# Performance work log

Hardware: AMD Instinct MI355X
Metric: run time of the kernel (lower is better)

Reference implementation:

```python
import jax, jax.numpy as jnp
import numpy as np

NUM_CLASSES = 2
OVERLAP_THRESHOLD = 0.35
NEG_POS_RATIO = 7
VARIANCES = (0.1, 0.2)
B, P, G = 16, 131072, 32


def point_form(pri):
    # center form (cx,cy,w,h) -> corner form (x1,y1,x2,y2)
    return jnp.concatenate([pri[:, :2] - pri[:, 2:] / 2,
                            pri[:, :2] + pri[:, 2:] / 2], axis=1)


def jaccard(box_a, box_b):
    # box_a [G,4], box_b [P,4], corner form -> IoU [G,P]
    max_xy = jnp.minimum(box_a[:, None, 2:], box_b[None, :, 2:])
    min_xy = jnp.maximum(box_a[:, None, :2], box_b[None, :, :2])
    inter = jnp.prod(jnp.clip(max_xy - min_xy, 0.0, None), axis=2)
    area_a = jnp.prod(box_a[:, 2:] - box_a[:, :2], axis=1)[:, None]
    area_b = jnp.prod(box_b[:, 2:] - box_b[:, :2], axis=1)[None, :]
    return inter / (area_a + area_b - inter)


def encode(matched, pri, variances):
    g_cxcy = ((matched[:, :2] + matched[:, 2:]) / 2 - pri[:, :2]) / (variances[0] * pri[:, 2:])
    g_wh = jnp.log((matched[:, 2:] - matched[:, :2]) / pri[:, 2:]) / variances[1]
    return jnp.concatenate([g_cxcy, g_wh], axis=1)


def encode_landm(matched, pri, variances):
    m = matched.reshape(-1, 5, 2)  # [P,5,2]
    g = (m - pri[:, None, :2]) / (variances[0] * pri[:, None, 2:])
    return g.reshape(-1, 10)


def match_one(truths, landms, labels, pri):
    overlaps = jaccard(truths, point_form(pri))          # [G,P]
    best_prior_idx = jnp.argmax(overlaps, axis=1)        # [G] best prior per gt
    best_truth_overlap = jnp.max(overlaps, axis=0)       # [P]
    best_truth_idx = jnp.argmax(overlaps, axis=0)        # [P]
    # ensure each gt keeps its best prior
    best_truth_overlap = best_truth_overlap.at[best_prior_idx].set(2.0)
    best_truth_idx = best_truth_idx.at[best_prior_idx].set(jnp.arange(truths.shape[0]))
    matches = truths[best_truth_idx]                     # [P,4]
    conf = jnp.where(best_truth_overlap < OVERLAP_THRESHOLD, 0, labels[best_truth_idx])
    loc = encode(matches, pri, VARIANCES)
    landm = encode_landm(landms[best_truth_idx], pri, VARIANCES)
    return loc, conf, landm


def smooth_l1(pred, gt):
    d = jnp.abs(pred - gt)
    return jnp.where(d < 1.0, 0.5 * d * d, d - 0.5)


def multibox_loss(conf_data, loc_data, landm_data, priors, targets):
    batch_size, num_priors = loc_data.shape[0], priors.shape[0]
    truths = targets[:, :, :4]
    landms = targets[:, :, 4:14]
    labels = targets[:, :, 14].astype(jnp.int32)
    loc_t, conf_t, landm_t = jax.vmap(lambda t, l, lb: match_one(t, l, lb, priors))(truths, landms, labels)

    pos = conf_t > 0                                      # [B,P]
    num_pos_total = jnp.maximum(pos.sum().astype(loc_data.dtype), 1.0)
    num_pos_per_image = pos.sum(axis=1, keepdims=True)    # [B,1]
    posf = pos.astype(loc_data.dtype)

    loss_box = (smooth_l1(loc_data, loc_t).sum(-1) * posf).sum()
    loss_landm = (smooth_l1(landm_data, landm_t).sum(-1) * posf).sum()

    logp = jax.nn.log_softmax(conf_data, axis=-1)         # [B,P,C]
    ce = -jnp.take_along_axis(logp, jnp.clip(conf_t, 0, None)[..., None], axis=-1)[..., 0]
    loss_c = jnp.where(pos | (conf_t < 0), 0.0, ce)       # zero pos & ignored
    # hard negative mining: rank by descending loss via double argsort
    loss_idx = jnp.argsort(-loss_c, axis=1)
    idx_rank = jnp.argsort(loss_idx, axis=1)
    num_neg = jnp.minimum(NEG_POS_RATIO * num_pos_per_image, num_priors - 1)
    neg = idx_rank < num_neg
    pn = (pos | neg).astype(conf_data.dtype)
    loss_c_final = (ce * pn).sum()
    return (loss_box / num_pos_total, loss_c_final / num_pos_total, loss_landm / num_pos_total)


def setup_inputs() -> dict:
    key = jax.random.key(0)
    k1, k2, k3, k4, k5, k6, k7 = jax.random.split(key, 7)
    conf_data = jax.random.normal(k1, (B, P, NUM_CLASSES), dtype=jnp.float32)
    loc_data = jax.random.normal(k2, (B, P, 4), dtype=jnp.float32)
    landm_data = jax.random.normal(k3, (B, P, 10), dtype=jnp.float32)
    # priors in center form
    pc = jax.random.uniform(k4, (P, 2), minval=0.0, maxval=1.0)
    pwh = jax.random.uniform(k5, (P, 2), minval=0.02, maxval=0.3)
    priors = jnp.concatenate([pc, pwh], axis=1).astype(jnp.float32)
    # targets: [B,G,15] = corner box(4) + landms(10) + label(1)
    c = jax.random.uniform(k6, (B, G, 2), minval=0.2, maxval=0.8)
    s = jax.random.uniform(k7, (B, G, 2), minval=0.05, maxval=0.3)
    box = jnp.concatenate([c - s / 2, c + s / 2], axis=-1)
    lm = jax.random.uniform(jax.random.fold_in(key, 99), (B, G, 10), minval=0.0, maxval=1.0)
    lbl = jnp.ones((B, G, 1), dtype=jnp.float32)
    targets = jnp.concatenate([box, lm, lbl], axis=-1).astype(jnp.float32)
    return {"conf_data": conf_data, "loc_data": loc_data, "landm_data": landm_data,
            "priors": priors, "targets": targets}


def reference(conf_data, loc_data, landm_data, priors, targets):
    return multibox_loss(conf_data, loc_data, landm_data, priors, targets)
```

## Files before the change

### kernel.cpp

```cpp
#include <hip/hip_runtime.h>
#include <math.h>

#define B_ 16
#define P_ 131072
#define G_ 32
constexpr float OVER_THR = 0.35f;
constexpr float VAR0 = 0.1f;
constexpr float VAR1 = 0.2f;
constexpr int NEG_POS = 7;
constexpr int UNR = 8;
constexpr int LOSS_X = P_ / 256;
constexpr int LOSS_BLOCKS = LOSS_X * B_;
constexpr int NBIN13 = 8192;
constexpr int NBIN8 = 256;
constexpr int NBIN11 = 2048;
constexpr int SCAN_BLKS = 16;

__device__ inline float s1(float d) {
    d = fabsf(d);
    return d < 1.f ? 0.5f * d * d : d - 0.5f;
}

__device__ inline unsigned long long shfl_xor_u64(unsigned long long x, int m) {
    unsigned lo = (unsigned)x, hi = (unsigned)(x >> 32);
    lo = __shfl_xor(lo, m);
    hi = __shfl_xor(hi, m);
    return ((unsigned long long)hi << 32) | lo;
}

template <int NB>
__device__ void topk_select(const unsigned* __restrict__ h, unsigned rem,
                            int* out_bin, unsigned* out_rem) {
    constexpr int CHUNK = NB / 256;
    const int tid = threadIdx.x;
    unsigned cnt[CHUNK];
    unsigned csum = 0;
#pragma unroll
    for (int j = 0; j < CHUNK; ++j) { cnt[j] = h[tid * CHUNK + j]; csum += cnt[j]; }
    __shared__ unsigned ss[256];
    ss[tid] = csum;
    __syncthreads();
    for (int off = 1; off < 256; off <<= 1) {
        unsigned other = (tid + off < 256) ? ss[tid + off] : 0u;
        __syncthreads();
        ss[tid] += other;
        __syncthreads();
    }
    unsigned incl = ss[tid];
    unsigned excl = incl - csum;
    if (excl < rem && incl >= rem) {
        unsigned r = rem - excl, cum = 0;
        int selbin = tid * CHUNK;
#pragma unroll
        for (int j = CHUNK - 1; j >= 0; --j) {
            unsigned c = cnt[j];
            if (cum + c >= r) { selbin = tid * CHUNK + j; r = r - cum; break; }
            cum += c;
        }
        *out_bin = selbin;
        *out_rem = r;
    }
}

__global__ __launch_bounds__(256, 3) void k_match(
        const float4* __restrict__ priors4, const float* __restrict__ targets,
        float* __restrict__ bt_ov, unsigned char* __restrict__ bt_idx,
        unsigned long long* __restrict__ pack) {
    const int b = blockIdx.y;
    const int base = blockIdx.x * (256 * UNR);
    const int tid = threadIdx.x;
    __shared__ float tb[G_][5];
    __shared__ unsigned long long red[G_][4];
    if (tid < G_ * 4) {
        int g = tid >> 2, j = tid & 3;
        tb[g][j] = targets[((size_t)b * G_ + g) * 15 + j];
    }
    __syncthreads();
    if (tid < G_) tb[tid][4] = (tb[tid][2] - tb[tid][0]) * (tb[tid][3] - tb[tid][1]);
    __syncthreads();

    float px1[UNR], py1[UNR], px2[UNR], py2[UNR], pap[UNR], best[UNR];
    int bidx[UNR];
#pragma unroll
    for (int j = 0; j < UNR; ++j) {
        float4 pr = priors4[base + j * 256 + tid];
        px1[j] = pr.x - pr.z * 0.5f;  py1[j] = pr.y - pr.w * 0.5f;
        px2[j] = pr.x + pr.z * 0.5f;  py2[j] = pr.y + pr.w * 0.5f;
        pap[j] = pr.z * pr.w;
        best[j] = -1.0f; bidx[j] = 0;
    }
    const int lane = tid & 63, wave = tid >> 6;
#pragma unroll 1
    for (int g = 0; g < G_; ++g) {
        float t0 = tb[g][0], t1 = tb[g][1], t2 = tb[g][2], t3 = tb[g][3], ta = tb[g][4];
        float gb = -1.0f; int gj = 0;
#pragma unroll
        for (int j = 0; j < UNR; ++j) {
            float iw = fminf(t2, px2[j]) - fmaxf(t0, px1[j]);
            float ih = fminf(t3, py2[j]) - fmaxf(t1, py1[j]);
            float inter = fmaxf(iw, 0.f) * fmaxf(ih, 0.f);
            float iou = inter * __builtin_amdgcn_rcpf(ta + pap[j] - inter);
            if (iou > best[j]) { best[j] = iou; bidx[j] = g; }
            if (iou > gb) { gb = iou; gj = j; }
        }
        unsigned p = (unsigned)(base + (gj << 8) + tid);
        unsigned long long pk =
            ((unsigned long long)__float_as_uint(gb) << 32) | (unsigned)(~p);
#pragma unroll
        for (int off = 32; off > 0; off >>= 1) {
            unsigned long long o = shfl_xor_u64(pk, off);
            if (o > pk) pk = o;
        }
        if (lane == 0) red[g][wave] = pk;
    }
    __syncthreads();
    if (tid < G_) {
        unsigned long long m = red[tid][0];
#pragma unroll
        for (int w = 1; w < 4; ++w) if (red[tid][w] > m) m = red[tid][w];
        atomicMax(&pack[b * G_ + tid], m);
    }
#pragma unroll
    for (int j = 0; j < UNR; ++j) {
        int p = base + j * 256 + tid;
        size_t o = (size_t)b * P_ + p;
        bt_ov[o] = best[j];
        bt_idx[o] = (unsigned char)bidx[j];
    }
}

__global__ void k_override(const unsigned long long* __restrict__ pack,
                           float* __restrict__ bt_ov, unsigned char* __restrict__ bt_idx) {
    int b = threadIdx.x;
    if (b >= B_) return;
    for (int g = 0; g < G_; ++g) {
        unsigned long long pk = pack[b * G_ + g];
        unsigned p = ~(unsigned)(pk & 0xFFFFFFFFull);
        if (p < P_) {
            bt_ov[(size_t)b * P_ + p] = 2.0f;
            bt_idx[(size_t)b * P_ + p] = (unsigned char)g;
        }
    }
}

__global__ __launch_bounds__(256) void k_loss(
        const float2* __restrict__ conf2, const float4* __restrict__ loc4,
        const float* __restrict__ landm, const float4* __restrict__ priors4,
        const float* __restrict__ targets,
        const float* __restrict__ bt_ov, const unsigned char* __restrict__ bt_idx,
        float* __restrict__ ce_neg,
        double* __restrict__ pb, double* __restrict__ pl,
        double* __restrict__ pc, int* __restrict__ pn) {
    const int b = blockIdx.y;
    const int p = blockIdx.x * 256 + threadIdx.x;
    const int tid = threadIdx.x;
    __shared__ float tg[G_ * 15];
    for (int i = tid; i < G_ * 15; i += 256) tg[i] = targets[(size_t)b * G_ * 15 + i];
    __syncthreads();

    const size_t gp = (size_t)b * P_ + p;
    float ov = bt_ov[gp];
    int ti = bt_idx[gp];
    const float* t = &tg[ti * 15];
    float label = t[14];
    int conf_t = (ov < OVER_THR) ? 0 : (int)label;
    bool pos = conf_t > 0;
    int cls = conf_t > 0 ? conf_t : 0;

    float2 c2 = conf2[gp];
    float mx = fmaxf(c2.x, c2.y);
    float lse = mx + logf(expf(c2.x - mx) + expf(c2.y - mx));
    float ce = lse - (cls ? c2.y : c2.x);
    ce_neg[gp] = (!pos && conf_t >= 0) ? ce : 0.f;

    float lb = 0.f, ll = 0.f;
    if (pos) {
        float4 pr = priors4[p];
        float vx = VAR0 * pr.z, vy = VAR0 * pr.w;
        float g0 = ((t[0] + t[2]) * 0.5f - pr.x) / vx;
        float g1 = ((t[1] + t[3]) * 0.5f - pr.y) / vy;
        float g2 = logf((t[2] - t[0]) / pr.z) / VAR1;
        float g3 = logf((t[3] - t[1]) / pr.w) / VAR1;
        float4 ld = loc4[gp];
        lb = s1(ld.x - g0) + s1(ld.y - g1) + s1(ld.z - g2) + s1(ld.w - g3);
        const float* lmp = landm + gp * 10;
#pragma unroll
        for (int i = 0; i < 5; ++i) {
            float2 lm = *(const float2*)(lmp + 2 * i);
            ll += s1(lm.x - (t[4 + 2 * i] - pr.x) / vx)
                + s1(lm.y - (t[5 + 2 * i] - pr.y) / vy);
        }
    }
    double vb = lb, vl = ll, vc = pos ? (double)ce : 0.0;
    int vp = pos ? 1 : 0;
#pragma unroll
    for (int off = 32; off > 0; off >>= 1) {
        vb += __shfl_xor(vb, off);
        vl += __shfl_xor(vl, off);
        vc += __shfl_xor(vc, off);
        vp += __shfl_xor(vp, off);
    }
    __shared__ double rb[4], rl[4], rc[4];
    __shared__ int rp[4];
    int lane = tid & 63, wave = tid >> 6;
    if (lane == 0) { rb[wave] = vb; rl[wave] = vl; rc[wave] = vc; rp[wave] = vp; }
    __syncthreads();
    if (tid == 0) {
        double sb = 0, sl = 0, sc = 0; int sp = 0;
        for (int w = 0; w < 4; ++w) { sb += rb[w]; sl += rl[w]; sc += rc[w]; sp += rp[w]; }
        int bi = blockIdx.y * LOSS_X + blockIdx.x;
        pb[bi] = sb; pl[bi] = sl; pc[bi] = sc; pn[bi] = sp;
    }
}

__global__ __launch_bounds__(1024) void k_hist13(
        const float* __restrict__ ce_neg, unsigned* __restrict__ hist) {
    const int b = blockIdx.y;
    const int tid = threadIdx.x;
    __shared__ unsigned h[NBIN13];
    for (int i = tid; i < NBIN13; i += 1024) h[i] = 0;
    __syncthreads();
    const float4* v4 = (const float4*)(ce_neg + (size_t)b * P_);
    const int c4 = P_ / SCAN_BLKS / 4;
    const int s4 = blockIdx.x * c4;
    for (int i = s4 + tid; i < s4 + c4; i += 1024) {
        float4 x = v4[i];
        atomicAdd(&h[__float_as_uint(x.x) >> 19], 1u);
        atomicAdd(&h[__float_as_uint(x.y) >> 19], 1u);
        atomicAdd(&h[__float_as_uint(x.z) >> 19], 1u);
        atomicAdd(&h[__float_as_uint(x.w) >> 19], 1u);
    }
    __syncthreads();
    unsigned* gh = hist + b * NBIN13;
    for (int i = tid; i < NBIN13; i += 1024)
        if (h[i]) atomicAdd(&gh[i], h[i]);
}

__global__ __launch_bounds__(256) void k_sel13(
        const unsigned* __restrict__ hist, const int* __restrict__ pn,
        int* __restrict__ sel, int* __restrict__ remk, int* __restrict__ npos) {
    const int b = blockIdx.x;
    const int tid = threadIdx.x;
    __shared__ int s_np;
    __shared__ int rnp[4];
    int loc = 0;
    for (int i = tid; i < LOSS_X; i += 256) loc += pn[b * LOSS_X + i];
#pragma unroll
    for (int off = 32; off > 0; off >>= 1) loc += __shfl_xor(loc, off);
    int lane = tid & 63, wave = tid >> 6;
    if (lane == 0) rnp[wave] = loc;
    __syncthreads();
    if (tid == 0) { int s = rnp[0] + rnp[1] + rnp[2] + rnp[3]; s_np = s; npos[b] = s; }
    __syncthreads();
    long long k = (long long)NEG_POS * s_np;
    if (k > P_ - 1) k = P_ - 1;
    if (k <= 0) { if (tid == 0) sel[b] = -1; return; }

    __shared__ int s_bin;
    __shared__ unsigned s_rem;
    topk_select<NBIN13>(hist + b * NBIN13, (unsigned)k, &s_bin, &s_rem);
    __syncthreads();
    if (tid == 0) { sel[b] = s_bin; remk[b] = (int)s_rem; }
}

__global__ __launch_bounds__(1024) void k_hist8(
        const float* __restrict__ ce_neg, const int* __restrict__ sel,
        unsigned* __restrict__ hist8) {
    const int b = blockIdx.y;
    const int s13 = sel[b];
    if (s13 < 0) return;
    const int tid = threadIdx.x;
    __shared__ unsigned h[NBIN8];
    if (tid < NBIN8) h[tid] = 0;
    __syncthreads();
    const float4* v4 = (const float4*)(ce_neg + (size_t)b * P_);
    const int c4 = P_ / SCAN_BLKS / 4;
    const int s4 = blockIdx.x * c4;
    for (int i = s4 + tid; i < s4 + c4; i += 1024) {
        float4 x = v4[i];
        unsigned u0 = __float_as_uint(x.x), u1 = __float_as_uint(x.y);
        unsigned u2 = __float_as_uint(x.z), u3 = __float_as_uint(x.w);
        if ((int)(u0 >> 19) == s13) atomicAdd(&h[(u0 >> 11) & 255u], 1u);
        if ((int)(u1 >> 19) == s13) atomicAdd(&h[(u1 >> 11) & 255u], 1u);
        if ((int)(u2 >> 19) == s13) atomicAdd(&h[(u2 >> 11) & 255u], 1u);
        if ((int)(u3 >> 19) == s13) atomicAdd(&h[(u3 >> 11) & 255u], 1u);
    }
    __syncthreads();
    if (tid < NBIN8 && h[tid]) atomicAdd(&hist8[b * NBIN8 + tid], h[tid]);
}

__global__ __launch_bounds__(256) void k_sel8(
        const unsigned* __restrict__ hist8, const int* __restrict__ sel,
        unsigned* __restrict__ pref, int* __restrict__ remk) {
    const int b = blockIdx.x;
    if (sel[b] < 0) return;
    __shared__ int s_bin;
    __shared__ unsigned s_rem;
    topk_select<NBIN8>(hist8 + b * NBIN8, (unsigned)remk[b], &s_bin, &s_rem);
    __syncthreads();
    if (threadIdx.x == 0) {
        pref[b] = ((unsigned)sel[b] << 8) | (unsigned)s_bin;
        remk[b] = (int)s_rem;
    }
}

__global__ __launch_bounds__(1024) void k_hist11(
        const float* __restrict__ ce_neg, const int* __restrict__ sel,
        const unsigned* __restrict__ pref, unsigned* __restrict__ hist11) {
    const int b = blockIdx.y;
    if (sel[b] < 0) return;
    const unsigned pf = pref[b];
    const int tid = threadIdx.x;
    __shared__ unsigned h[NBIN11];
    for (int i = tid; i < NBIN11; i += 1024) h[i] = 0;
    __syncthreads();
    const float4* v4 = (const float4*)(ce_neg + (size_t)b * P_);
    const int c4 = P_ / SCAN_BLKS / 4;
    const int s4 = blockIdx.x * c4;
    for (int i = s4 + tid; i < s4 + c4; i += 1024) {
        float4 x = v4[i];
        unsigned u0 = __float_as_uint(x.x), u1 = __float_as_uint(x.y);
        unsigned u2 = __float_as_uint(x.z), u3 = __float_as_uint(x.w);
        if ((u0 >> 11) == pf) atomicAdd(&h[u0 & 2047u], 1u);
        if ((u1 >> 11) == pf) atomicAdd(&h[u1 & 2047u], 1u);
        if ((u2 >> 11) == pf) atomicAdd(&h[u2 & 2047u], 1u);
        if ((u3 >> 11) == pf) atomicAdd(&h[u3 & 2047u], 1u);
    }
    __syncthreads();
    unsigned* gh = hist11 + b * NBIN11;
    for (int i = tid; i < NBIN11; i += 1024)
        if (h[i]) atomicAdd(&gh[i], h[i]);
}

__global__ __launch_bounds__(256) void k_sel11(
        const unsigned* __restrict__ hist11, const int* __restrict__ sel,
        const unsigned* __restrict__ pref, const int* __restrict__ remk,
        unsigned* __restrict__ thr, double* __restrict__ tot) {
    const int b = blockIdx.x;
    if (sel[b] < 0) { if (threadIdx.x == 0) thr[b] = 0xFFFFFFFFu; return; }
    __shared__ int s_bin;
    __shared__ unsigned s_rem;
    topk_select<NBIN11>(hist11 + b * NBIN11, (unsigned)remk[b], &s_bin, &s_rem);
    __syncthreads();
    if (threadIdx.x == 0) {
        unsigned t = (pref[b] << 11) | (unsigned)s_bin;
        thr[b] = t;
        atomicAdd(&tot[2], (double)s_rem * (double)__uint_as_float(t));
    }
}

__global__ __launch_bounds__(1024) void k_sumtop(
        const float* __restrict__ ce_neg, const unsigned* __restrict__ thr,
        double* __restrict__ tot) {
    const int b = blockIdx.y;
    const unsigned t = thr[b];
    if (t == 0xFFFFFFFFu) return;
    const int tid = threadIdx.x;
    const float4* v4 = (const float4*)(ce_neg + (size_t)b * P_);
    const int c4 = P_ / SCAN_BLKS / 4;
    const int s4 = blockIdx.x * c4;
    double loc = 0;
    for (int i = s4 + tid; i < s4 + c4; i += 1024) {
        float4 x = v4[i];
        if (__float_as_uint(x.x) > t) loc += x.x;
        if (__float_as_uint(x.y) > t) loc += x.y;
        if (__float_as_uint(x.z) > t) loc += x.z;
        if (__float_as_uint(x.w) > t) loc += x.w;
    }
#pragma unroll
    for (int off = 32; off > 0; off >>= 1) loc += __shfl_xor(loc, off);
    __shared__ double rs[16];
    int lane = tid & 63, wave = tid >> 6;
    if (lane == 0) rs[wave] = loc;
    __syncthreads();
    if (tid == 0) {
        double s = 0;
        for (int w = 0; w < 16; ++w) s += rs[w];
        atomicAdd(&tot[2], s);
    }
}

__global__ __launch_bounds__(1024) void k_final(
        const double* __restrict__ pb, const double* __restrict__ pl,
        const double* __restrict__ pc, const int* __restrict__ npos,
        const double* __restrict__ tot, float* __restrict__ out) {
    int tid = threadIdx.x;
    double sb = 0, sl = 0, sc = 0;
    for (int i = tid; i < LOSS_BLOCKS; i += 1024) {
        sb += pb[i]; sl += pl[i]; sc += pc[i];
    }
#pragma unroll
    for (int off = 32; off > 0; off >>= 1) {
        sb += __shfl_xor(sb, off);
        sl += __shfl_xor(sl, off);
        sc += __shfl_xor(sc, off);
    }
    __shared__ double rb[16], rl[16], rc[16];
    int lane = tid & 63, wave = tid >> 6;
    if (lane == 0) { rb[wave] = sb; rl[wave] = sl; rc[wave] = sc; }
    __syncthreads();
    if (tid == 0) {
        double b2 = 0, l2 = 0, c2 = 0;
        for (int w = 0; w < 16; ++w) { b2 += rb[w]; l2 += rl[w]; c2 += rc[w]; }
        long long tp = 0;
        for (int b = 0; b < B_; ++b) tp += npos[b];
        double n = tp > 0 ? (double)tp : 1.0;
        out[0] = (float)(b2 / n);
        out[1] = (float)((c2 + tot[2]) / n);
        out[2] = (float)(l2 / n);
    }
}

extern "C" void kernel_launch(void* const* d_in, const int* in_sizes, int n_in,
                              void* d_out, int out_size, void* d_ws, size_t ws_size,
                              hipStream_t stream) {
    const float* conf    = (const float*)d_in[0];
    const float* loc     = (const float*)d_in[1];
    const float* landm   = (const float*)d_in[2];
    const float* priors  = (const float*)d_in[3];
    const float* targets = (const float*)d_in[4];

    char* ws = (char*)d_ws;
    double* tot = (double*)ws;
    int* npos = (int*)(ws + 64);
    int* sel  = (int*)(ws + 128);
    int* remk = (int*)(ws + 192);
    unsigned* pref = (unsigned*)(ws + 256);
    unsigned* thr  = (unsigned*)(ws + 320);
    unsigned long long* pack = (unsigned long long*)(ws + 512);
    unsigned* hist13 = (unsigned*)(ws + 4608);
    unsigned* hist8  = hist13 + (size_t)B_ * NBIN13;
    unsigned* hist11 = hist8 + (size_t)B_ * NBIN8;
    size_t zero_bytes = 4608 + (size_t)B_ * (NBIN13 + NBIN8 + NBIN11) * 4;
    size_t big = (zero_bytes + 255) & ~(size_t)255;
    size_t BP = (size_t)B_ * P_;
    float* bt_ov = (float*)(ws + big);
    unsigned char* bt_idx = (unsigned char*)(ws + big + BP * 4);
    float* ce_neg = (float*)(ws + big + BP * 5);
    char* part = ws + big + BP * 9;
    double* pb = (double*)part;
    double* pl = (double*)(part + LOSS_BLOCKS * 8);
    double* pc = (double*)(part + LOSS_BLOCKS * 16);
    int*    pn = (int*)(part + LOSS_BLOCKS * 24);

    hipMemsetAsync(ws, 0, zero_bytes, stream);
    k_match<<<dim3(P_ / (256 * UNR), B_), 256, 0, stream>>>(
        (const float4*)priors, targets, bt_ov, bt_idx, pack);
    k_override<<<1, 64, 0, stream>>>(pack, bt_ov, bt_idx);
    k_loss<<<dim3(LOSS_X, B_), 256, 0, stream>>>(
        (const float2*)conf, (const float4*)loc, landm, (const float4*)priors,
        targets, bt_ov, bt_idx, ce_neg, pb, pl, pc, pn);
    k_hist13<<<dim3(SCAN_BLKS, B_), 1024, 0, stream>>>(ce_neg, hist13);
    k_sel13<<<B_, 256, 0, stream>>>(hist13, pn, sel, remk, npos);
    k_hist8<<<dim3(SCAN_BLKS, B_), 1024, 0, stream>>>(ce_neg, sel, hist8);
    k_sel8<<<B_, 256, 0, stream>>>(hist8, sel, pref, remk);
    k_hist11<<<dim3(SCAN_BLKS, B_), 1024, 0, stream>>>(ce_neg, sel, pref, hist11);
    k_sel11<<<B_, 256, 0, stream>>>(hist11, sel, pref, remk, thr, tot);
    k_sumtop<<<dim3(SCAN_BLKS, B_), 1024, 0, stream>>>(ce_neg, thr, tot);
    k_final<<<1, 1024, 0, stream>>>(pb, pl, pc, npos, tot, (float*)d_out);
}
```

Baseline: 127.4 us.

## Compact candidate-bin elements after first radix pass to shrink later top-k passes

After the first 13-bit histogram selects the threshold bin, a new kernel sums all values above that bin and compacts the elements inside the bin into a per-batch buffer. A single-block-per-batch kernel then runs the 8-bit and 11-bit refinement histograms and the final partial sum over only the compacted elements. Three full passes over ce_neg and four launches are replaced by one scan plus one small kernel. The cost is per-element shared atomics for compaction slots, extra workspace, and serial work in one block per batch if the candidate bin is large.

```diff
diff --git a/kernel.cpp b/kernel.cpp
--- a/kernel.cpp
+++ b/kernel.cpp
@@ -263,109 +263,47 @@
     if (tid == 0) { sel[b] = s_bin; remk[b] = (int)s_rem; }
 }
 
-__global__ __launch_bounds__(1024) void k_hist8(
+__global__ __launch_bounds__(1024) void k_compact(
         const float* __restrict__ ce_neg, const int* __restrict__ sel,
-        unsigned* __restrict__ hist8) {
+        int* __restrict__ cnt, float* __restrict__ compact,
+        double* __restrict__ tot) {
     const int b = blockIdx.y;
     const int s13 = sel[b];
     if (s13 < 0) return;
     const int tid = threadIdx.x;
-    __shared__ unsigned h[NBIN8];
-    if (tid < NBIN8) h[tid] = 0;
+    __shared__ unsigned lcnt, gbase, lc2;
+    if (tid == 0) { lcnt = 0; lc2 = 0; }
     __syncthreads();
     const float4* v4 = (const float4*)(ce_neg + (size_t)b * P_);
     const int c4 = P_ / SCAN_BLKS / 4;
     const int s4 = blockIdx.x * c4;
+    double loc = 0;
+    unsigned nloc = 0;
     for (int i = s4 + tid; i < s4 + c4; i += 1024) {
         float4 x = v4[i];
         unsigned u0 = __float_as_uint(x.x), u1 = __float_as_uint(x.y);
         unsigned u2 = __float_as_uint(x.z), u3 = __float_as_uint(x.w);
-        if ((int)(u0 >> 19) == s13) atomicAdd(&h[(u0 >> 11) & 255u], 1u);
-        if ((int)(u1 >> 19) == s13) atomicAdd(&h[(u1 >> 11) & 255u], 1u);
-        if ((int)(u2 >> 19) == s13) atomicAdd(&h[(u2 >> 11) & 255u], 1u);
-        if ((int)(u3 >> 19) == s13) atomicAdd(&h[(u3 >> 11) & 255u], 1u);
-    }
-    __syncthreads();
-    if (tid < NBIN8 && h[tid]) atomicAdd(&hist8[b * NBIN8 + tid], h[tid]);
-}
-
-__global__ __launch_bounds__(256) void k_sel8(
-        const unsigned* __restrict__ hist8, const int* __restrict__ sel,
-        unsigned* __restrict__ pref, int* __restrict__ remk) {
-    const int b = blockIdx.x;
-    if (sel[b] < 0) return;
-    __shared__ int s_bin;
-    __shared__ unsigned s_rem;
-    topk_select<NBIN8>(hist8 + b * NBIN8, (unsigned)remk[b], &s_bin, &s_rem);
-    __syncthreads();
-    if (threadIdx.x == 0) {
-        pref[b] = ((unsigned)sel[b] << 8) | (unsigned)s_bin;
-        remk[b] = (int)s_rem;
-    }
-}
-
-__global__ __launch_bounds__(1024) void k_hist11(
-        const float* __restrict__ ce_neg, const int* __restrict__ sel,
-        const unsigned* __restrict__ pref, unsigned* __restrict__ hist11) {
-    const int b = blockIdx.y;
-    if (sel[b] < 0) return;
-    const unsigned pf = pref[b];
-    const int tid = threadIdx.x;
-    __shared__ unsigned h[NBIN11];
-    for (int i = tid; i < NBIN11; i += 1024) h[i] = 0;
-    __syncthreads();
-    const float4* v4 = (const float4*)(ce_neg + (size_t)b * P_);
-    const int c4 = P_ / SCAN_BLKS / 4;
-    const int s4 = blockIdx.x * c4;
+        if ((int)(u0 >> 19) > s13) loc += x.x; else if ((int)(u0 >> 19) == s13) nloc++;
+        if ((int)(u1 >> 19) > s13) loc += x.y; else if ((int)(u1 >> 19) == s13) nloc++;
+        if ((int)(u2 >> 19) > s13) loc += x.z; else if ((int)(u2 >> 19) == s13) nloc++;
+        if ((int)(u3 >> 19) > s13) loc += x.w; else if ((int)(u3 >> 19) == s13) nloc++;
+    }
+    unsigned nw = nloc;
+#pragma unroll
+    for (int off = 32; off > 0; off >>= 1) nw += __shfl_xor(nw, off);
+    if ((tid & 63) == 0 && nw) atomicAdd(&lcnt, nw);
+    __syncthreads();
+    if (tid == 0) gbase = atomicAdd((unsigned*)&cnt[b], lcnt);
+    __syncthreads();
+    float* dst = compact + (size_t)b * P_;
     for (int i = s4 + tid; i < s4 + c4; i += 1024) {
         float4 x = v4[i];
         unsigned u0 = __float_as_uint(x.x), u1 = __float_as_uint(x.y);
         unsigned u2 = __float_as_uint(x.z), u3 = __float_as_uint(x.w);
-        if ((u0 >> 11) == pf) atomicAdd(&h[u0 & 2047u], 1u);
-        if ((u1 >> 11) == pf) atomicAdd(&h[u1 & 2047u], 1u);
-        if ((u2 >> 11) == pf) atomicAdd(&h[u2 & 2047u], 1u);
-        if ((u3 >> 11) == pf) atomicAdd(&h[u3 & 2047u], 1u);
-    }
-    __syncthreads();
-    unsigned* gh = hist11 + b * NBIN11;
-    for (int i = tid; i < NBIN11; i += 1024)
-        if (h[i]) atomicAdd(&gh[i], h[i]);
-}
-
-__global__ __launch_bounds__(256) void k_sel11(
-        const unsigned* __restrict__ hist11, const int* __restrict__ sel,
-        const unsigned* __restrict__ pref, const int* __restrict__ remk,
-        unsigned* __restrict__ thr, double* __restrict__ tot) {
-    const int b = blockIdx.x;
-    if (sel[b] < 0) { if (threadIdx.x == 0) thr[b] = 0xFFFFFFFFu; return; }
-    __shared__ int s_bin;
-    __shared__ unsigned s_rem;
-    topk_select<NBIN11>(hist11 + b * NBIN11, (unsigned)remk[b], &s_bin, &s_rem);
-    __syncthreads();
-    if (threadIdx.x == 0) {
-        unsigned t = (pref[b] << 11) | (unsigned)s_bin;
-        thr[b] = t;
-        atomicAdd(&tot[2], (double)s_rem * (double)__uint_as_float(t));
-    }
-}
-
-__global__ __launch_bounds__(1024) void k_sumtop(
-        const float* __restrict__ ce_neg, const unsigned* __restrict__ thr,
-        double* __restrict__ tot) {
-    const int b = blockIdx.y;
-    const unsigned t = thr[b];
-    if (t == 0xFFFFFFFFu) return;
-    const int tid = threadIdx.x;
-    const float4* v4 = (const float4*)(ce_neg + (size_t)b * P_);
-    const int c4 = P_ / SCAN_BLKS / 4;
-    const int s4 = blockIdx.x * c4;
-    double loc = 0;
-    for (int i = s4 + tid; i < s4 + c4; i += 1024) {
-        float4 x = v4[i];
-        if (__float_as_uint(x.x) > t) loc += x.x;
-        if (__float_as_uint(x.y) > t) loc += x.y;
-        if (__float_as_uint(x.z) > t) loc += x.z;
-        if (__float_as_uint(x.w) > t) loc += x.w;
+        if ((int)(u0 >> 19) == s13) dst[gbase + atomicAdd(&lc2, 1u)] = x.x;
+        if ((int)(u1 >> 19) == s13) dst[gbase + atomicAdd(&lc2, 1u)] = x.y;
+        if ((int)(u2 >> 19) == s13) dst[gbase + atomicAdd(&lc2, 1u)] = x.z;
+        if ((int)(u3 >> 19) == s13) dst[gbase + atomicAdd(&lc2, 1u)] = x.w;
     }
 #pragma unroll
     for (int off = 32; off > 0; off >>= 1) loc += __shfl_xor(loc, off);
@@ -376,6 +314,65 @@
     if (tid == 0) {
         double s = 0;
         for (int w = 0; w < 16; ++w) s += rs[w];
+        atomicAdd(&tot[2], s);
+    }
+}
+
+__global__ __launch_bounds__(256) void k_fin(
+        const float* __restrict__ compact, const int* __restrict__ cnt,
+        const int* __restrict__ sel, const int* __restrict__ remk,
+        double* __restrict__ tot) {
+    const int b = blockIdx.x;
+    const int s13 = sel[b];
+    if (s13 < 0) return;
+    const int tid = threadIdx.x;
+    const int n = cnt[b];
+    const float* src = compact + (size_t)b * P_;
+    unsigned rem = (unsigned)remk[b];
+
+    __shared__ unsigned h8[NBIN8];
+    if (tid < NBIN8) h8[tid] = 0;
+    __syncthreads();
+    for (int i = tid; i < n; i += 256) {
+        unsigned u = __float_as_uint(src[i]);
+        atomicAdd(&h8[(u >> 11) & 255u], 1u);
+    }
+    __syncthreads();
+    __shared__ int sb8;
+    __shared__ unsigned sr8;
+    topk_select<NBIN8>(h8, rem, &sb8, &sr8);
+    __syncthreads();
+    const unsigned pf = ((unsigned)s13 << 8) | (unsigned)sb8;
+    rem = sr8;
+
+    __shared__ unsigned h11[NBIN11];
+    for (int i = tid; i < NBIN11; i += 256) h11[i] = 0;
+    __syncthreads();
+    for (int i = tid; i < n; i += 256) {
+        unsigned u = __float_as_uint(src[i]);
+        if ((u >> 11) == pf) atomicAdd(&h11[u & 2047u], 1u);
+    }
+    __syncthreads();
+    __shared__ int sb11;
+    __shared__ unsigned sr11;
+    topk_select<NBIN11>(h11, rem, &sb11, &sr11);
+    __syncthreads();
+    const unsigned T = (pf << 11) | (unsigned)sb11;
+
+    double loc = 0;
+    for (int i = tid; i < n; i += 256) {
+        float x = src[i];
+        if (__float_as_uint(x) > T) loc += x;
+    }
+#pragma unroll
+    for (int off = 32; off > 0; off >>= 1) loc += __shfl_xor(loc, off);
+    __shared__ double rs[4];
+    int lane = tid & 63, wave = tid >> 6;
+    if (lane == 0) rs[wave] = loc;
+    __syncthreads();
+    if (tid == 0) {
+        double s = rs[0] + rs[1] + rs[2] + rs[3];
+        s += (double)sr11 * (double)__uint_as_float(T);
         atomicAdd(&tot[2], s);
     }
 }
@@ -425,19 +422,17 @@
     int* npos = (int*)(ws + 64);
     int* sel  = (int*)(ws + 128);
     int* remk = (int*)(ws + 192);
-    unsigned* pref = (unsigned*)(ws + 256);
-    unsigned* thr  = (unsigned*)(ws + 320);
+    int* cnt  = (int*)(ws + 256);
     unsigned long long* pack = (unsigned long long*)(ws + 512);
     unsigned* hist13 = (unsigned*)(ws + 4608);
-    unsigned* hist8  = hist13 + (size_t)B_ * NBIN13;
-    unsigned* hist11 = hist8 + (size_t)B_ * NBIN8;
-    size_t zero_bytes = 4608 + (size_t)B_ * (NBIN13 + NBIN8 + NBIN11) * 4;
+    size_t zero_bytes = 4608 + (size_t)B_ * NBIN13 * 4;
     size_t big = (zero_bytes + 255) & ~(size_t)255;
     size_t BP = (size_t)B_ * P_;
     float* bt_ov = (float*)(ws + big);
     unsigned char* bt_idx = (unsigned char*)(ws + big + BP * 4);
     float* ce_neg = (float*)(ws + big + BP * 5);
-    char* part = ws + big + BP * 9;
+    float* compact = (float*)(ws + big + BP * 9);
+    char* part = ws + big + BP * 13;
     double* pb = (double*)part;
     double* pl = (double*)(part + LOSS_BLOCKS * 8);
     double* pc = (double*)(part + LOSS_BLOCKS * 16);
@@ -452,10 +447,7 @@
         targets, bt_ov, bt_idx, ce_neg, pb, pl, pc, pn);
     k_hist13<<<dim3(SCAN_BLKS, B_), 1024, 0, stream>>>(ce_neg, hist13);
     k_sel13<<<B_, 256, 0, stream>>>(hist13, pn, sel, remk, npos);
-    k_hist8<<<dim3(SCAN_BLKS, B_), 1024, 0, stream>>>(ce_neg, sel, hist8);
-    k_sel8<<<B_, 256, 0, stream>>>(hist8, sel, pref, remk);
-    k_hist11<<<dim3(SCAN_BLKS, B_), 1024, 0, stream>>>(ce_neg, sel, pref, hist11);
-    k_sel11<<<B_, 256, 0, stream>>>(hist11, sel, pref, remk, thr, tot);
-    k_sumtop<<<dim3(SCAN_BLKS, B_), 1024, 0, stream>>>(ce_neg, thr, tot);
+    k_compact<<<dim3(SCAN_BLKS, B_), 1024, 0, stream>>>(ce_neg, sel, cnt, compact, tot);
+    k_fin<<<B_, 256, 0, stream>>>(compact, cnt, sel, remk, tot);
     k_final<<<1, 1024, 0, stream>>>(pb, pl, pc, npos, tot, (float*)d_out);
 }
```

New measurement: 173.0 us. +35.8%, slower.

## Pack match index and threshold flag into one byte; read targets directly

Applied to the files above, without the earlier changes.

Replaces the per-prior float overlap plus byte index intermediate with a single byte holding the matched-truth index and a flag for passing the overlap threshold. This removes a 4-byte-per-prior write in k_match and read in k_loss across B*P elements. It also drops the shared-memory staging of target boxes in k_match, reading them from global memory inside the loop instead and recomputing the area. That removes two block barriers but adds uniform global loads per truth box.

```diff
diff --git a/kernel.cpp b/kernel.cpp
--- a/kernel.cpp
+++ b/kernel.cpp
@@ -64,20 +64,11 @@
 
 __global__ __launch_bounds__(256, 3) void k_match(
         const float4* __restrict__ priors4, const float* __restrict__ targets,
-        float* __restrict__ bt_ov, unsigned char* __restrict__ bt_idx,
-        unsigned long long* __restrict__ pack) {
+        unsigned char* __restrict__ bt, unsigned long long* __restrict__ pack) {
     const int b = blockIdx.y;
     const int base = blockIdx.x * (256 * UNR);
     const int tid = threadIdx.x;
-    __shared__ float tb[G_][5];
     __shared__ unsigned long long red[G_][4];
-    if (tid < G_ * 4) {
-        int g = tid >> 2, j = tid & 3;
-        tb[g][j] = targets[((size_t)b * G_ + g) * 15 + j];
-    }
-    __syncthreads();
-    if (tid < G_) tb[tid][4] = (tb[tid][2] - tb[tid][0]) * (tb[tid][3] - tb[tid][1]);
-    __syncthreads();
 
     float px1[UNR], py1[UNR], px2[UNR], py2[UNR], pap[UNR], best[UNR];
     int bidx[UNR];
@@ -90,9 +81,12 @@
         best[j] = -1.0f; bidx[j] = 0;
     }
     const int lane = tid & 63, wave = tid >> 6;
+    const float* tgb = targets + (size_t)b * G_ * 15;
 #pragma unroll 1
     for (int g = 0; g < G_; ++g) {
-        float t0 = tb[g][0], t1 = tb[g][1], t2 = tb[g][2], t3 = tb[g][3], ta = tb[g][4];
+        const float* tp = tgb + g * 15;
+        float t0 = tp[0], t1 = tp[1], t2 = tp[2], t3 = tp[3];
+        float ta = (t2 - t0) * (t3 - t1);
         float gb = -1.0f; int gj = 0;
 #pragma unroll
         for (int j = 0; j < UNR; ++j) {
@@ -123,23 +117,19 @@
 #pragma unroll
     for (int j = 0; j < UNR; ++j) {
         int p = base + j * 256 + tid;
-        size_t o = (size_t)b * P_ + p;
-        bt_ov[o] = best[j];
-        bt_idx[o] = (unsigned char)bidx[j];
+        bt[(size_t)b * P_ + p] =
+            (unsigned char)(bidx[j] | (best[j] >= OVER_THR ? 64 : 0));
     }
 }
 
 __global__ void k_override(const unsigned long long* __restrict__ pack,
-                           float* __restrict__ bt_ov, unsigned char* __restrict__ bt_idx) {
+                           unsigned char* __restrict__ bt) {
     int b = threadIdx.x;
     if (b >= B_) return;
     for (int g = 0; g < G_; ++g) {
         unsigned long long pk = pack[b * G_ + g];
         unsigned p = ~(unsigned)(pk & 0xFFFFFFFFull);
-        if (p < P_) {
-            bt_ov[(size_t)b * P_ + p] = 2.0f;
-            bt_idx[(size_t)b * P_ + p] = (unsigned char)g;
-        }
+        if (p < P_) bt[(size_t)b * P_ + p] = (unsigned char)(g | 64);
     }
 }
 
@@ -147,7 +137,7 @@
         const float2* __restrict__ conf2, const float4* __restrict__ loc4,
         const float* __restrict__ landm, const float4* __restrict__ priors4,
         const float* __restrict__ targets,
-        const float* __restrict__ bt_ov, const unsigned char* __restrict__ bt_idx,
+        const unsigned char* __restrict__ bt,
         float* __restrict__ ce_neg,
         double* __restrict__ pb, double* __restrict__ pl,
         double* __restrict__ pc, int* __restrict__ pn) {
@@ -159,11 +149,12 @@
     __syncthreads();
 
     const size_t gp = (size_t)b * P_ + p;
-    float ov = bt_ov[gp];
-    int ti = bt_idx[gp];
+    unsigned char bv = bt[gp];
+    int ti = bv & 63;
+    bool thr_ok = (bv & 64) != 0;
     const float* t = &tg[ti * 15];
     float label = t[14];
-    int conf_t = (ov < OVER_THR) ? 0 : (int)label;
+    int conf_t = thr_ok ? (int)label : 0;
     bool pos = conf_t > 0;
     int cls = conf_t > 0 ? conf_t : 0;
 
@@ -434,10 +425,9 @@
     size_t zero_bytes = 4608 + (size_t)B_ * (NBIN13 + NBIN8 + NBIN11) * 4;
     size_t big = (zero_bytes + 255) & ~(size_t)255;
     size_t BP = (size_t)B_ * P_;
-    float* bt_ov = (float*)(ws + big);
-    unsigned char* bt_idx = (unsigned char*)(ws + big + BP * 4);
-    float* ce_neg = (float*)(ws + big + BP * 5);
-    char* part = ws + big + BP * 9;
+    unsigned char* bt = (unsigned char*)(ws + big);
+    float* ce_neg = (float*)(ws + big + BP);
+    char* part = ws + big + BP * 5;
     double* pb = (double*)part;
     double* pl = (double*)(part + LOSS_BLOCKS * 8);
     double* pc = (double*)(part + LOSS_BLOCKS * 16);
@@ -445,11 +435,11 @@
 
     hipMemsetAsync(ws, 0, zero_bytes, stream);
     k_match<<<dim3(P_ / (256 * UNR), B_), 256, 0, stream>>>(
-        (const float4*)priors, targets, bt_ov, bt_idx, pack);
-    k_override<<<1, 64, 0, stream>>>(pack, bt_ov, bt_idx);
+        (const float4*)priors, targets, bt, pack);
+    k_override<<<1, 64, 0, stream>>>(pack, bt);
     k_loss<<<dim3(LOSS_X, B_), 256, 0, stream>>>(
         (const float2*)conf, (const float4*)loc, landm, (const float4*)priors,
-        targets, bt_ov, bt_idx, ce_neg, pb, pl, pc, pn);
+        targets, bt, ce_neg, pb, pl, pc, pn);
     k_hist13<<<dim3(SCAN_BLKS, B_), 1024, 0, stream>>>(ce_neg, hist13);
     k_sel13<<<B_, 256, 0, stream>>>(hist13, pn, sel, remk, npos);
     k_hist8<<<dim3(SCAN_BLKS, B_), 1024, 0, stream>>>(ce_neg, sel, hist8);
```

Result: no change. 128.0 us (+0.5%).
